# Kernel tuning notes

Measured on AMD Instinct MI355X. Metric: run time of the kernel, lower is better.

The kernel has to match this reference:

```python
import jax, jax.numpy as jnp
import numpy as np

T, B, D, H = 512, 32, 512, 256
A1, A2, O = 16, 128, 1

def setup_inputs() -> dict:
    key = jax.random.key(0)
    ks = jax.random.split(key, 15)
    s = 0.1  # scale params so exp() attention stays well-conditioned
    return {
        "inputs": jax.random.normal(ks[0], (T, B, D), jnp.float32),
        "W1": jax.random.normal(ks[1], (1, A1), jnp.float32) * s,
        "b1": jax.random.normal(ks[2], (A1,), jnp.float32) * s,
        "u1": jax.random.normal(ks[3], (A1, 1), jnp.float32) * s,
        "W_ih": jax.random.normal(ks[4], (4 * H, 1), jnp.float32) * s,
        "W_hh": jax.random.normal(ks[5], (4 * H, H), jnp.float32) * s,
        "b_ih": jax.random.normal(ks[6], (4 * H,), jnp.float32) * s,
        "b_hh": jax.random.normal(ks[7], (4 * H,), jnp.float32) * s,
        "h0": jax.random.normal(ks[8], (B, H), jnp.float32),
        "c0": jax.random.uniform(ks[9], (B, H), jnp.float32),
        "W2": jax.random.normal(ks[10], (H, A2), jnp.float32) * s,
        "b2": jax.random.normal(ks[11], (A2,), jnp.float32) * s,
        "u2": jax.random.normal(ks[12], (A2, 1), jnp.float32) * s,
        "Wl": jax.random.normal(ks[13], (O, H), jnp.float32) * s,
        "bl": jax.random.normal(ks[14], (O,), jnp.float32) * s,
    }

def reference(inputs, W1, b1, u1, W_ih, W_hh, b_ih, b_hh, h0, c0, W2, b2, u2, Wl, bl):
    # --- AttLayer1: soft pooling over feature axis D ---
    x = inputs[..., None]                       # (T,B,D,1)
    uit = jnp.tanh(x @ W1 + b1)                 # (T,B,D,A1)
    ait = jnp.exp(jnp.squeeze(uit @ u1, -1))    # (T,B,D)  (matches torch.exp, no max-subtract)
    ait = ait / jnp.sum(ait, axis=2, keepdims=True)
    seq = jnp.sum(x * ait[..., None], axis=2)   # (T,B,1)

    # --- per-step LSTM (PyTorch gate order i,f,g,o), state detached each step ---
    def step(carry, x_t):
        h, c = carry
        h = jax.lax.stop_gradient(h)            # mirrors .detach() between steps
        c = jax.lax.stop_gradient(c)
        gates = x_t @ W_ih.T + b_ih + h @ W_hh.T + b_hh  # (B,4H)
        i, f, g, o = jnp.split(gates, 4, axis=-1)
        c_new = jax.nn.sigmoid(f) * c + jax.nn.sigmoid(i) * jnp.tanh(g)
        h_new = jax.nn.sigmoid(o) * jnp.tanh(c_new)
        return (h_new, c_new), h_new

    _, hs = jax.lax.scan(step, (h0, c0), seq)   # hs: (T,B,H)

    # --- AttLayer2: soft pooling over time axis T ---
    uit2 = jnp.tanh(hs @ W2 + b2)               # (T,B,A2)
    a2 = jnp.exp(jnp.squeeze(uit2 @ u2, -1))    # (T,B)
    a2 = a2 / jnp.sum(a2, axis=0, keepdims=True)
    pooled = jnp.sum(hs * a2[..., None], axis=0)  # (B,H)

    # --- final linear head ---
    return pooled @ Wl.T + bl                   # (B,1)
```

## Files before the change

### kernel.cpp

```cpp
#include <hip/hip_runtime.h>
#include <hip/hip_fp16.h>

constexpr int kT = 512, kB = 32, kD = 512, kH = 256, kA1 = 16, kA2 = 128;

typedef _Float16 h2_t __attribute__((ext_vector_type(2)));
typedef _Float16 h8_t __attribute__((ext_vector_type(8)));
typedef unsigned u4_t __attribute__((ext_vector_type(4)));

#if defined(__has_builtin)
#if __has_builtin(__builtin_amdgcn_fdot2)
#define HAVE_FDOT2 1
#endif
#endif

__device__ __forceinline__ float fast_tanh(float x) {
    float e = __expf(2.0f * x);
    return 1.0f - 2.0f / (e + 1.0f);
}
__device__ __forceinline__ float fast_sig(float x) {
    return 1.0f / (1.0f + __expf(-x));
}

__device__ __forceinline__ float dot_pair(h2_t w, h2_t h, float acc) {
#if defined(HAVE_FDOT2)
    return __builtin_amdgcn_fdot2(w, h, acc, false);
#else
    acc = fmaf((float)w[0], (float)h[0], acc);
    return fmaf((float)w[1], (float)h[1], acc);
#endif
}

__global__ __launch_bounds__(256) void att1_kernel(
    const float* __restrict__ x, const float* __restrict__ W1,
    const float* __restrict__ b1, const float* __restrict__ u1,
    float* __restrict__ seq) {
    int blk = blockIdx.x;
    int tid = threadIdx.x;
    const float* xp = x + (size_t)blk * kD;
    float x0 = xp[tid], x1 = xp[tid + 256];
    float s0 = 0.f, s1 = 0.f;
#pragma unroll
    for (int a = 0; a < kA1; ++a) {
        float w = W1[a], bb = b1[a], uu = u1[a];
        s0 += fast_tanh(fmaf(x0, w, bb)) * uu;
        s1 += fast_tanh(fmaf(x1, w, bb)) * uu;
    }
    float e0 = __expf(s0), e1 = __expf(s1);
    float se = e0 + e1;
    float sxe = fmaf(x0, e0, x1 * e1);
#pragma unroll
    for (int m = 32; m; m >>= 1) {
        se  += __shfl_xor(se,  m, 64);
        sxe += __shfl_xor(sxe, m, 64);
    }
    __shared__ float r_se[4], r_sxe[4];
    int wave = tid >> 6, lane = tid & 63;
    if (lane == 0) { r_se[wave] = se; r_sxe[wave] = sxe; }
    __syncthreads();
    if (tid == 0) {
        float S = r_se[0] + r_se[1] + r_se[2] + r_se[3];
        float X = r_sxe[0] + r_sxe[1] + r_sxe[2] + r_sxe[3];
        seq[blk] = X / S;
    }
}

__global__ __launch_bounds__(256) void wconv_kernel(
    const float* __restrict__ Whh, _Float16* __restrict__ WQ) {
    int idx = blockIdx.x * 256 + threadIdx.x;
    int j = idx >> 7, kk = idx & 127;
    int kk4 = kk >> 2, q = kk & 3;
    float a = Whh[j * kH + 2 * kk];
    float b = Whh[j * kH + 2 * kk + 1];
    _Float16* dst = WQ + ((size_t)kk4 * 8192 + j * 8 + q * 2);
    dst[0] = (_Float16)a;
    dst[1] = (_Float16)b;
}

#define LSTM_BARRIER() asm volatile("s_waitcnt lgkmcnt(0)\n\ts_barrier" ::: "memory")

#define HPAIR(KK) __builtin_bit_cast(h2_t, (unsigned)__builtin_amdgcn_readlane( \
        ((KK) < 64) ? (int)hr0 : (int)hr1, (KK) & 63))

#define DOT4(W0, W1, KKB) do { \
    h2_t _hp0 = HPAIR((KKB) + 0); \
    acc0 = dot_pair(__builtin_shufflevector((W0), (W0), 0, 1), _hp0, acc0); \
    acc1 = dot_pair(__builtin_shufflevector((W1), (W1), 0, 1), _hp0, acc1); \
    h2_t _hp1 = HPAIR((KKB) + 1); \
    acc0 = dot_pair(__builtin_shufflevector((W0), (W0), 2, 3), _hp1, acc0); \
    acc1 = dot_pair(__builtin_shufflevector((W1), (W1), 2, 3), _hp1, acc1); \
    h2_t _hp2 = HPAIR((KKB) + 2); \
    acc0 = dot_pair(__builtin_shufflevector((W0), (W0), 4, 5), _hp2, acc0); \
    acc1 = dot_pair(__builtin_shufflevector((W1), (W1), 4, 5), _hp2, acc1); \
    h2_t _hp3 = HPAIR((KKB) + 3); \
    acc0 = dot_pair(__builtin_shufflevector((W0), (W0), 6, 7), _hp3, acc0); \
    acc1 = dot_pair(__builtin_shufflevector((W1), (W1), 6, 7), _hp3, acc1); \
} while (0)

__global__ __launch_bounds__(512, 2) void lstm_kernel(
    const float* __restrict__ seq, const _Float16* __restrict__ WQ,
    const float* __restrict__ W_ih, const float* __restrict__ b_ih,
    const float* __restrict__ b_hh, const float* __restrict__ h0,
    const float* __restrict__ c0, float* __restrict__ hs) {
    int b = blockIdx.x;
    int j = threadIdx.x;
    int lane = j & 63;

    __shared__ float seq_l[kT];
    __shared__ __align__(16) _Float16 wtail[8 * 1024 * 8];
    __shared__ float fo[2][kH];
    __shared__ __align__(8) _Float16 hl[kH];

    const u4_t* W4 = (const u4_t*)WQ;

    u4_t wr0[24], wr1[24];
#pragma unroll
    for (int kk4 = 0; kk4 < 24; ++kk4) {
        const u4_t* p0 = W4 + kk4 * 1024 + j;
        const u4_t* p1 = p0 + 512;
        asm volatile("global_load_dwordx4 %0, %1, off" : "=v"(wr0[kk4]) : "v"(p0));
        asm volatile("global_load_dwordx4 %0, %1, off" : "=v"(wr1[kk4]) : "v"(p1));
    }

    for (int t = j; t < kT; t += 512) seq_l[t] = seq[t * kB + b];

    u4_t* wt4 = (u4_t*)wtail;
    for (int idx = j; idx < 8 * 1024; idx += 512)
        wt4[idx] = W4[(24 + (idx >> 10)) * 1024 + (idx & 1023)];

    int r0 = j, r1 = j + 512;
    float wih0 = W_ih[r0], wih1 = W_ih[r1];
    float bias0 = b_ih[r0] + b_hh[r0];
    float bias1 = b_ih[r1] + b_hh[r1];
    float c = 0.f;
    if (j < kH) {
        c = c0[b * kH + j];
        hl[j] = (_Float16)h0[b * kH + j];
    }
    asm volatile("s_waitcnt vmcnt(0)" ::: "memory");
    __builtin_amdgcn_sched_barrier(0);
    LSTM_BARRIER();

    const unsigned* hl32 = (const unsigned*)hl;
    unsigned hr0 = hl32[lane];
    unsigned hr1 = hl32[lane + 64];

#pragma unroll 1
    for (int t = 0; t < kT; ++t) {
        float st = seq_l[t];
        float acc0 = fmaf(st, wih0, bias0);
        float acc1 = fmaf(st, wih1, bias1);

#pragma unroll
        for (int kk4 = 0; kk4 < 24; ++kk4) {
            h8_t w0 = __builtin_bit_cast(h8_t, wr0[kk4]);
            h8_t w1 = __builtin_bit_cast(h8_t, wr1[kk4]);
            DOT4(w0, w1, kk4 * 4);
        }
#pragma unroll 2
        for (int q = 0; q < 8; ++q) {
            h8_t w0 = __builtin_bit_cast(h8_t, wt4[q * 1024 + j]);
            h8_t w1 = __builtin_bit_cast(h8_t, wt4[q * 1024 + j + 512]);
            DOT4(w0, w1, 96 + q * 4);
        }

        if (j >= kH) {
            fo[0][j - kH] = acc0;
            fo[1][j - kH] = acc1;
        }
        LSTM_BARRIER();

        if (j < kH) {
            float ig = fast_sig(acc0);
            float gg = fast_tanh(acc1);
            float fg = fast_sig(fo[0][j]);
            float og = fast_sig(fo[1][j]);
            c = fmaf(fg, c, ig * gg);
            float h = og * fast_tanh(c);
            hs[(size_t)t * (kB * kH) + b * kH + j] = h;
            hl[j] = (_Float16)h;
        }
        LSTM_BARRIER();

        hr0 = hl32[lane];
        hr1 = hl32[lane + 64];
    }
}

__global__ __launch_bounds__(128) void att2a_kernel(
    const float* __restrict__ hs, const float* __restrict__ W2,
    const float* __restrict__ b2, const float* __restrict__ u2,
    float* __restrict__ a2w) {
    int b  = blockIdx.x & 31;
    int tc = blockIdx.x >> 5;
    int a  = threadIdx.x;
    __shared__ __align__(16) float hl[16][kH];
    __shared__ float red[16][2];
    int t0 = tc * 16;
    for (int tt = 0; tt < 16; ++tt) {
        const float* hp = hs + ((size_t)(t0 + tt) * kB + b) * kH;
        hl[tt][a]       = hp[a];
        hl[tt][a + 128] = hp[a + 128];
    }
    __syncthreads();
    float dot[16];
#pragma unroll
    for (int tt = 0; tt < 16; ++tt) dot[tt] = 0.f;
    for (int k = 0; k < kH; k += 4) {
        float w0 = W2[(k + 0) * kA2 + a];
        float w1 = W2[(k + 1) * kA2 + a];
        float w2 = W2[(k + 2) * kA2 + a];
        float w3 = W2[(k + 3) * kA2 + a];
#pragma unroll
        for (int tt = 0; tt < 16; ++tt) {
            float4 h4 = *(const float4*)&hl[tt][k];
            dot[tt] = fmaf(h4.x, w0, dot[tt]);
            dot[tt] = fmaf(h4.y, w1, dot[tt]);
            dot[tt] = fmaf(h4.z, w2, dot[tt]);
            dot[tt] = fmaf(h4.w, w3, dot[tt]);
        }
    }
    float bb = b2[a], uu = u2[a];
    int wave = a >> 6, lane = a & 63;
#pragma unroll
    for (int tt = 0; tt < 16; ++tt) {
        float v = fast_tanh(dot[tt] + bb) * uu;
#pragma unroll
        for (int m = 32; m; m >>= 1) v += __shfl_xor(v, m, 64);
        if (lane == 0) red[tt][wave] = v;
    }
    __syncthreads();
    if (a < 16) {
        float s = red[a][0] + red[a][1];
        a2w[(t0 + a) * kB + b] = __expf(s);
    }
}

__global__ __launch_bounds__(256) void att2b_kernel(
    const float* __restrict__ hs, const float* __restrict__ a2w,
    const float* __restrict__ Wl, const float* __restrict__ bl,
    float* __restrict__ out) {
    int b = blockIdx.x;
    int k = threadIdx.x;
    float acc = 0.f, den = 0.f;
    for (int t = 0; t < kT; ++t) {
        float e = a2w[t * kB + b];
        float h = hs[((size_t)t * kB + b) * kH + k];
        acc = fmaf(h, e, acc);
        den += e;
    }
    float v = (acc / den) * Wl[k];
#pragma unroll
    for (int m = 32; m; m >>= 1) v += __shfl_xor(v, m, 64);
    __shared__ float red[4];
    int wave = k >> 6, lane = k & 63;
    if (lane == 0) red[wave] = v;
    __syncthreads();
    if (k == 0) out[b] = red[0] + red[1] + red[2] + red[3] + bl[0];
}

extern "C" void kernel_launch(void* const* d_in, const int* in_sizes, int n_in,
                              void* d_out, int out_size, void* d_ws, size_t ws_size,
                              hipStream_t stream) {
    const float* inputs = (const float*)d_in[0];
    const float* W1   = (const float*)d_in[1];
    const float* b1   = (const float*)d_in[2];
    const float* u1   = (const float*)d_in[3];
    const float* W_ih = (const float*)d_in[4];
    const float* W_hh = (const float*)d_in[5];
    const float* b_ih = (const float*)d_in[6];
    const float* b_hh = (const float*)d_in[7];
    const float* h0   = (const float*)d_in[8];
    const float* c0   = (const float*)d_in[9];
    const float* W2   = (const float*)d_in[10];
    const float* b2   = (const float*)d_in[11];
    const float* u2   = (const float*)d_in[12];
    const float* Wl   = (const float*)d_in[13];
    const float* bl   = (const float*)d_in[14];
    float* out = (float*)d_out;

    char* ws = (char*)d_ws;
    float*    seq = (float*)(ws);
    float*    a2w = (float*)(ws + (64 << 10));
    _Float16* WQ  = (_Float16*)(ws + (128 << 10));
    float*    hs  = (float*)(ws + (1 << 20));

    att1_kernel <<<kT * kB, 256, 0, stream>>>(inputs, W1, b1, u1, seq);
    wconv_kernel<<<512, 256, 0, stream>>>(W_hh, WQ);
    lstm_kernel <<<kB, 512, 0, stream>>>(seq, WQ, W_ih, b_ih, b_hh, h0, c0, hs);
    att2a_kernel<<<1024, 128, 0, stream>>>(hs, W2, b2, u2, a2w);
    att2b_kernel<<<kB, 256, 0, stream>>>(hs, a2w, Wl, bl, out);
}
```

Before: 1.438 ms.

## Use 1024 threads per LSTM block with one gate row per thread

Each LSTM block now runs 1024 threads, each computing a single gate row instead of two, and the register-resident weight slice per thread is halved. All four gate pre-activations go through a shared gates array read by the first 256 threads. This shortens the per-thread serial dot-product chain on each timestep. In exchange it adds more waves per barrier and more LDS traffic, and the explicit asm loads plus the vmcnt wait are replaced by plain loads.

After: 1.603 ms. +11.5%, slower.

```diff
diff --git a/kernel.cpp b/kernel.cpp
--- a/kernel.cpp
+++ b/kernel.cpp
@@ -80,23 +80,23 @@
 
 #define HPAIR(KK) __builtin_bit_cast(h2_t, (unsigned)__builtin_amdgcn_readlane( \
         ((KK) < 64) ? (int)hr0 : (int)hr1, (KK) & 63))
-
-#define DOT4(W0, W1, KKB) do { \
-    h2_t _hp0 = HPAIR((KKB) + 0); \
-    acc0 = dot_pair(__builtin_shufflevector((W0), (W0), 0, 1), _hp0, acc0); \
-    acc1 = dot_pair(__builtin_shufflevector((W1), (W1), 0, 1), _hp0, acc1); \
-    h2_t _hp1 = HPAIR((KKB) + 1); \
-    acc0 = dot_pair(__builtin_shufflevector((W0), (W0), 2, 3), _hp1, acc0); \
-    acc1 = dot_pair(__builtin_shufflevector((W1), (W1), 2, 3), _hp1, acc1); \
-    h2_t _hp2 = HPAIR((KKB) + 2); \
-    acc0 = dot_pair(__builtin_shufflevector((W0), (W0), 4, 5), _hp2, acc0); \
-    acc1 = dot_pair(__builtin_shufflevector((W1), (W1), 4, 5), _hp2, acc1); \
-    h2_t _hp3 = HPAIR((KKB) + 3); \
-    acc0 = dot_pair(__builtin_shufflevector((W0), (W0), 6, 7), _hp3, acc0); \
-    acc1 = dot_pair(__builtin_shufflevector((W1), (W1), 6, 7), _hp3, acc1); \
+#define HPAIRT(KK) __builtin_bit_cast(h2_t, (unsigned)__builtin_amdgcn_readlane( \
+        (int)hr1, (KK) - 64))
+
+#define DOT4A(W, KKB) do { \
+    acc = dot_pair(__builtin_shufflevector((W), (W), 0, 1), HPAIR((KKB) + 0), acc); \
+    acc = dot_pair(__builtin_shufflevector((W), (W), 2, 3), HPAIR((KKB) + 1), acc); \
+    acc = dot_pair(__builtin_shufflevector((W), (W), 4, 5), HPAIR((KKB) + 2), acc); \
+    acc = dot_pair(__builtin_shufflevector((W), (W), 6, 7), HPAIR((KKB) + 3), acc); \
 } while (0)
-
-__global__ __launch_bounds__(512, 2) void lstm_kernel(
+#define DOT4AT(W, KKB) do { \
+    acc = dot_pair(__builtin_shufflevector((W), (W), 0, 1), HPAIRT((KKB) + 0), acc); \
+    acc = dot_pair(__builtin_shufflevector((W), (W), 2, 3), HPAIRT((KKB) + 1), acc); \
+    acc = dot_pair(__builtin_shufflevector((W), (W), 4, 5), HPAIRT((KKB) + 2), acc); \
+    acc = dot_pair(__builtin_shufflevector((W), (W), 6, 7), HPAIRT((KKB) + 3), acc); \
+} while (0)
+
+__global__ __launch_bounds__(1024, 4) void lstm_kernel(
     const float* __restrict__ seq, const _Float16* __restrict__ WQ,
     const float* __restrict__ W_ih, const float* __restrict__ b_ih,
     const float* __restrict__ b_hh, const float* __restrict__ h0,
@@ -107,37 +107,29 @@
 
     __shared__ float seq_l[kT];
     __shared__ __align__(16) _Float16 wtail[8 * 1024 * 8];
-    __shared__ float fo[2][kH];
+    __shared__ float gates_l[4 * kH];
     __shared__ __align__(8) _Float16 hl[kH];
 
     const u4_t* W4 = (const u4_t*)WQ;
 
-    u4_t wr0[24], wr1[24];
-#pragma unroll
-    for (int kk4 = 0; kk4 < 24; ++kk4) {
-        const u4_t* p0 = W4 + kk4 * 1024 + j;
-        const u4_t* p1 = p0 + 512;
-        asm volatile("global_load_dwordx4 %0, %1, off" : "=v"(wr0[kk4]) : "v"(p0));
-        asm volatile("global_load_dwordx4 %0, %1, off" : "=v"(wr1[kk4]) : "v"(p1));
-    }
-
-    for (int t = j; t < kT; t += 512) seq_l[t] = seq[t * kB + b];
+    u4_t wr[24];
+#pragma unroll
+    for (int kk4 = 0; kk4 < 24; ++kk4)
+        wr[kk4] = W4[kk4 * 1024 + j];
+
+    for (int t = j; t < kT; t += 1024) seq_l[t] = seq[t * kB + b];
 
     u4_t* wt4 = (u4_t*)wtail;
-    for (int idx = j; idx < 8 * 1024; idx += 512)
+    for (int idx = j; idx < 8 * 1024; idx += 1024)
         wt4[idx] = W4[(24 + (idx >> 10)) * 1024 + (idx & 1023)];
 
-    int r0 = j, r1 = j + 512;
-    float wih0 = W_ih[r0], wih1 = W_ih[r1];
-    float bias0 = b_ih[r0] + b_hh[r0];
-    float bias1 = b_ih[r1] + b_hh[r1];
+    float wih  = W_ih[j];
+    float bias = b_ih[j] + b_hh[j];
     float c = 0.f;
     if (j < kH) {
         c = c0[b * kH + j];
         hl[j] = (_Float16)h0[b * kH + j];
     }
-    asm volatile("s_waitcnt vmcnt(0)" ::: "memory");
-    __builtin_amdgcn_sched_barrier(0);
     LSTM_BARRIER();
 
     const unsigned* hl32 = (const unsigned*)hl;
@@ -146,34 +138,27 @@
 
 #pragma unroll 1
     for (int t = 0; t < kT; ++t) {
-        float st = seq_l[t];
-        float acc0 = fmaf(st, wih0, bias0);
-        float acc1 = fmaf(st, wih1, bias1);
+        float acc = fmaf(seq_l[t], wih, bias);
 
 #pragma unroll
         for (int kk4 = 0; kk4 < 24; ++kk4) {
-            h8_t w0 = __builtin_bit_cast(h8_t, wr0[kk4]);
-            h8_t w1 = __builtin_bit_cast(h8_t, wr1[kk4]);
-            DOT4(w0, w1, kk4 * 4);
+            h8_t w = __builtin_bit_cast(h8_t, wr[kk4]);
+            DOT4A(w, kk4 * 4);
         }
 #pragma unroll 2
         for (int q = 0; q < 8; ++q) {
-            h8_t w0 = __builtin_bit_cast(h8_t, wt4[q * 1024 + j]);
-            h8_t w1 = __builtin_bit_cast(h8_t, wt4[q * 1024 + j + 512]);
-            DOT4(w0, w1, 96 + q * 4);
-        }
-
-        if (j >= kH) {
-            fo[0][j - kH] = acc0;
-            fo[1][j - kH] = acc1;
-        }
+            h8_t w = __builtin_bit_cast(h8_t, wt4[q * 1024 + j]);
+            DOT4AT(w, 96 + q * 4);
+        }
+
+        gates_l[j] = acc;
         LSTM_BARRIER();
 
         if (j < kH) {
-            float ig = fast_sig(acc0);
-            float gg = fast_tanh(acc1);
-            float fg = fast_sig(fo[0][j]);
-            float og = fast_sig(fo[1][j]);
+            float ig = fast_sig(acc);
+            float fg = fast_sig(gates_l[kH + j]);
+            float gg = fast_tanh(gates_l[2 * kH + j]);
+            float og = fast_sig(gates_l[3 * kH + j]);
             c = fmaf(fg, c, ig * gg);
             float h = og * fast_tanh(c);
             hs[(size_t)t * (kB * kH) + b * kH + j] = h;
@@ -286,7 +271,7 @@
 
     att1_kernel <<<kT * kB, 256, 0, stream>>>(inputs, W1, b1, u1, seq);
     wconv_kernel<<<512, 256, 0, stream>>>(W_hh, WQ);
-    lstm_kernel <<<kB, 512, 0, stream>>>(seq, WQ, W_ih, b_ih, b_hh, h0, c0, hs);
+    lstm_kernel <<<kB, 1024, 0, stream>>>(seq, WQ, W_ih, b_ih, b_hh, h0, c0, hs);
     att2a_kernel<<<1024, 128, 0, stream>>>(hs, W2, b2, u2, a2w);
     att2b_kernel<<<kB, 256, 0, stream>>>(hs, a2w, Wl, bl, out);
 }
```
